# Kernel optimization log

Hardware: AMD Instinct MI355X
Metric: run time of the kernel (lower is better)

The kernel has to match this reference:

```python
import jax, jax.numpy as jnp
import numpy as np

N_NODES = 100000
N_EDGES = 1600000
D_IN = 128
D_OUT = 128


def setup_inputs() -> dict:
    key = jax.random.key(0)
    k1, k2, k3, k4, k5, k6 = jax.random.split(key, 6)
    x = jax.random.normal(k1, (N_NODES, D_IN), dtype=jnp.float32)
    edge_src = jax.random.randint(k2, (N_EDGES,), 0, N_NODES, dtype=jnp.int64 if jax.config.jax_enable_x64 else jnp.int32)
    edge_dst = jax.random.randint(k3, (N_EDGES,), 0, N_NODES, dtype=jnp.int64 if jax.config.jax_enable_x64 else jnp.int32)
    edge_val = jax.random.uniform(k4, (N_EDGES,), dtype=jnp.float32)
    # nn.Linear(2*D_IN, D_OUT): store W as [2*D_IN, D_OUT] (transposed torch layout)
    W = jax.random.normal(k5, (2 * D_IN, D_OUT), dtype=jnp.float32) * (1.0 / np.sqrt(2 * D_IN))
    b = jax.random.normal(k6, (D_OUT,), dtype=jnp.float32) * 0.01
    return {"x": x, "edge_src": edge_src, "edge_dst": edge_dst, "edge_val": edge_val, "W": W, "b": b}


def reference(x, edge_src, edge_dst, edge_val, W, b):
    # support = adj @ x  (sparse COO: adj[dst, src] = edge_val)
    gathered = x[edge_src] * edge_val[:, None]               # [E, D_IN]
    support = jax.ops.segment_sum(gathered, edge_dst, num_segments=x.shape[0])  # [N, D_IN]
    # concat self + aggregated neighbor features, then linear
    h = jnp.concatenate([x, support], axis=1)                # [N, 2*D_IN]
    return h @ W + b                                          # [N, D_OUT]
```

## Files before the change

kernel.cpp:

```cpp
#include <hip/hip_runtime.h>

#define D 128
#define BN 64
#define NBIN 391
#define NBMAX 512
#define CHUNK 2048
#define SCAP 12

typedef __attribute__((ext_vector_type(8))) short bf16x8;
typedef __attribute__((ext_vector_type(4))) float f32x4;

__device__ __forceinline__ unsigned short f2bf(float f) {
    unsigned int u = __builtin_bit_cast(unsigned int, f);
    u = (u + 0x7fffu + ((u >> 16) & 1u)) >> 16;
    return (unsigned short)u;
}
__device__ __forceinline__ float bf2f(unsigned int u) {
    return __builtin_bit_cast(float, u << 16);
}

__global__ void prep_kernel(const float* __restrict__ x,
                            unsigned short* __restrict__ x_bf,
                            const float* __restrict__ W,
                            unsigned short* __restrict__ WT,
                            int* __restrict__ ccnt,
                            int n4, int XB, int WB) {
    int blk = blockIdx.x, tid = threadIdx.x;
    if (blk < XB) {
        int i = blk * 256 + tid;
        if (i < n4) {
            float4 v = ((const float4*)x)[i];
            ushort4 s;
            s.x = f2bf(v.x); s.y = f2bf(v.y); s.z = f2bf(v.z); s.w = f2bf(v.w);
            ((ushort4*)x_bf)[i] = s;
        }
    } else if (blk < XB + WB) {
        int t = (blk - XB) * 256 + tid;
        if (t < 2 * D * D) {
            int col = t & 127, k = t >> 7;
            WT[col * 256 + k] = f2bf(W[k * D + col]);
        }
    } else {
        ccnt[tid] = 0;
        ccnt[tid + 256] = 0;
    }
}

__global__ __launch_bounds__(256) void chist_kernel(const int* __restrict__ edst,
                                                    int* __restrict__ ccnt, int E) {
    __shared__ int h[NBMAX];
    for (int i = threadIdx.x; i < NBMAX; i += 256) h[i] = 0;
    __syncthreads();
    int stride = gridDim.x * 256;
    for (int e = blockIdx.x * 256 + threadIdx.x; e < E; e += stride)
        atomicAdd(&h[edst[e] >> 8], 1);
    __syncthreads();
    for (int i = threadIdx.x; i < NBIN; i += 256) {
        int c = h[i];
        if (c) atomicAdd(&ccnt[i], c);
    }
}

__global__ __launch_bounds__(256) void cscan_kernel(const int* __restrict__ ccnt,
                                                    int* __restrict__ cbase,
                                                    int* __restrict__ ccur) {
    __shared__ int p[256];
    int t = threadIdx.x;
    int s0 = ccnt[2 * t], s1 = ccnt[2 * t + 1];
    int loc = s0 + s1;
    p[t] = loc;
    __syncthreads();
    for (int off = 1; off < 256; off <<= 1) {
        int v = p[t];
        int u = (t >= off) ? p[t - off] : 0;
        __syncthreads();
        p[t] = v + u;
        __syncthreads();
    }
    int ex = p[t] - loc;
    cbase[2 * t] = ex;     ccur[2 * t] = ex;
    cbase[2 * t + 1] = ex + s0; ccur[2 * t + 1] = ex + s0;
}

__global__ __launch_bounds__(256) void cfill_kernel(const int* __restrict__ esrc,
                                                    const int* __restrict__ edst,
                                                    const float* __restrict__ eval,
                                                    int* __restrict__ ccur,
                                                    int2* __restrict__ ep, int E) {
    __shared__ int lh[NBMAX];
    __shared__ int lcur[NBMAX];
    __shared__ int p[256];
    __shared__ int2 ord[CHUNK];
    __shared__ unsigned short obk[CHUNK];

    const int tid = threadIdx.x;
    const int base = blockIdx.x * CHUNK;
    const int n = min(CHUNK, E - base);

    for (int i = tid; i < NBMAX; i += 256) lh[i] = 0;
    __syncthreads();

    int esv[8]; int ebk[8];
    float evv[8];
#pragma unroll
    for (int k = 0; k < 8; ++k) {
        int li = k * 256 + tid;
        if (li < n) {
            int i = base + li;
            int dst = edst[i];
            esv[k] = esrc[i];
            evv[k] = eval[i];
            int b = dst >> 8;
            ebk[k] = b | ((dst & 255) << 16);
            atomicAdd(&lh[b], 1);
        } else ebk[k] = -1;
    }
    __syncthreads();

    int s0 = lh[2 * tid], s1 = lh[2 * tid + 1];
    int loc = s0 + s1;
    p[tid] = loc;
    __syncthreads();
    for (int off = 1; off < 256; off <<= 1) {
        int v = p[tid];
        int u = (tid >= off) ? p[tid - off] : 0;
        __syncthreads();
        p[tid] = v + u;
        __syncthreads();
    }
    int ex = p[tid] - loc;
    lcur[2 * tid] = ex;
    lcur[2 * tid + 1] = ex + s0;
    __syncthreads();

#pragma unroll
    for (int k = 0; k < 8; ++k) {
        if (ebk[k] >= 0) {
            int b = ebk[k] & 0xffff, nl = ebk[k] >> 16;
            int slot = atomicAdd(&lcur[b], 1);
            ord[slot] = make_int2((esv[k] << 8) | nl, __builtin_bit_cast(int, evv[k]));
            obk[slot] = (unsigned short)b;
        }
    }
    __syncthreads();

    for (int b = tid; b < NBIN; b += 256) {
        int c = lh[b];
        if (c) lh[b] = atomicAdd(&ccur[b], c) - (lcur[b] - c);
    }
    __syncthreads();

    for (int i = tid; i < n; i += 256) {
        int b = obk[i];
        ep[lh[b] + i] = ord[i];
    }
}

__global__ __launch_bounds__(512) void csort_kernel(int2* __restrict__ ep,
                                                    const int* __restrict__ cbase,
                                                    const int* __restrict__ ccnt,
                                                    int* __restrict__ node_start) {
    __shared__ int h[256];
    __shared__ int p[256];

    const int t = threadIdx.x;
    const int bin = blockIdx.x;
    const int cb = cbase[bin];
    const int ce = cb + ccnt[bin];

    if (t < 256) h[t] = 0;
    __syncthreads();

    int2 ev[SCAP];
#pragma unroll
    for (int k = 0; k < SCAP; ++k) {
        int idx = cb + k * 512 + t;
        if (idx < ce) {
            int2 e = ep[idx];
            ev[k] = e;
            atomicAdd(&h[e.x & 255], 1);
        } else ev[k] = make_int2(-1, 0);
    }
    __syncthreads();

    int c = 0;
    if (t < 256) { c = h[t]; p[t] = c; }
    __syncthreads();
    for (int off = 1; off < 256; off <<= 1) {
        int v = 0, u = 0;
        if (t < 256) { v = p[t]; u = (t >= off) ? p[t - off] : 0; }
        __syncthreads();
        if (t < 256) p[t] = v + u;
        __syncthreads();
    }
    if (t < 256) {
        int st = cb + p[t] - c;
        node_start[bin * 256 + t] = st;
        h[t] = st;
    }
    __syncthreads();

#pragma unroll
    for (int k = 0; k < SCAP; ++k) {
        if (ev[k].x >= 0) {
            int nl = ev[k].x & 255;
            int pos = atomicAdd(&h[nl], 1);
            ep[pos] = make_int2(ev[k].x & 0xFFFFFF3F, ev[k].y);
        }
    }
}

__global__ __launch_bounds__(256, 8) void gather_fused_kernel(
        const unsigned short* __restrict__ x_bf,
        const int* __restrict__ node_start,
        const int2* __restrict__ edge_pack,
        const unsigned short* __restrict__ WT,
        const float* __restrict__ bias,
        float* __restrict__ out, int N) {
    __shared__ unsigned short accb[BN * 136];
    __shared__ int nb[BN + 1];

    const int tid = threadIdx.x;
    const int b = blockIdx.x;
    const int node0 = b * BN;
    const int w = tid >> 6, lane = tid & 63;
    unsigned int* accw = (unsigned int*)accb;

    for (int i = tid * 8; i < BN * 136; i += 2048)
        *(uint4*)(accb + i) = make_uint4(0u, 0u, 0u, 0u);
    if (tid <= BN) nb[tid] = node_start[node0 + tid];
    __syncthreads();

    const int js = __builtin_amdgcn_readfirstlane(nb[w * 16]);
    const int je = __builtin_amdgcn_readfirstlane(nb[w * 16 + 16]);
    const unsigned short* xl = x_bf + lane * 2;

    int cur = -1;
    float ax = 0.f, ay = 0.f;
    for (int g = js; g < je; g += 16) {
        int m = je - g; if (m > 16) m = 16;
        int2 e[16];
#pragma unroll
        for (int k = 0; k < 16; ++k) {
            int idx = g + k; if (idx >= je) idx = je - 1;
            e[k] = edge_pack[idx];
        }
        unsigned int p[16];
#pragma unroll
        for (int k = 0; k < 16; ++k)
            p[k] = *(const unsigned int*)(xl + ((e[k].x >> 8) << 7));
#pragma unroll
        for (int k = 0; k < 16; ++k) {
            if (k < m) {
                int nd = e[k].x & 63;
                if (nd != cur) {
                    if (cur >= 0)
                        accw[cur * 68 + lane] =
                            (unsigned int)f2bf(ax) | ((unsigned int)f2bf(ay) << 16);
                    cur = nd; ax = 0.f; ay = 0.f;
                }
                float v = __builtin_bit_cast(float, e[k].y);
                ax += bf2f(p[k] & 0xffffu) * v;
                ay += bf2f(p[k] >> 16) * v;
            }
        }
    }
    if (cur >= 0)
        accw[cur * 68 + lane] = (unsigned int)f2bf(ax) | ((unsigned int)f2bf(ay) << 16);
    __syncthreads();

    const int quad = lane >> 4;
    const int l15  = lane & 15;
    const int colbase = w * 32;

    f32x4 acc[4][2];
#pragma unroll
    for (int rt = 0; rt < 4; ++rt) {
        acc[rt][0] = (f32x4){0.f, 0.f, 0.f, 0.f};
        acc[rt][1] = (f32x4){0.f, 0.f, 0.f, 0.f};
    }

#pragma unroll
    for (int ks = 0; ks < 8; ++ks) {
        bf16x8 wf0 = *(const bf16x8*)(WT + (size_t)(colbase + l15) * 256 + ks * 32 + quad * 8);
        bf16x8 wf1 = *(const bf16x8*)(WT + (size_t)(colbase + 16 + l15) * 256 + ks * 32 + quad * 8);
#pragma unroll
        for (int rt = 0; rt < 4; ++rt) {
            int row = rt * 16 + l15;
            bf16x8 a;
            if (ks < 4) {
                int rg = node0 + row; if (rg >= N) rg = N - 1;
                a = *(const bf16x8*)(x_bf + (size_t)rg * D + ks * 32 + quad * 8);
            } else {
                a = *(const bf16x8*)(accb + row * 136 + (ks - 4) * 32 + quad * 8);
            }
            acc[rt][0] = __builtin_amdgcn_mfma_f32_16x16x32_bf16(a, wf0, acc[rt][0], 0, 0, 0);
            acc[rt][1] = __builtin_amdgcn_mfma_f32_16x16x32_bf16(a, wf1, acc[rt][1], 0, 0, 0);
        }
    }

#pragma unroll
    for (int ct = 0; ct < 2; ++ct) {
        int col = colbase + ct * 16 + l15;
        float bv = bias[col];
#pragma unroll
        for (int rt = 0; rt < 4; ++rt) {
#pragma unroll
            for (int rg = 0; rg < 4; ++rg) {
                int row = node0 + rt * 16 + quad * 4 + rg;
                if (row < N)
                    out[(size_t)row * D + col] = acc[rt][ct][rg] + bv;
            }
        }
    }
}

extern "C" void kernel_launch(void* const* d_in, const int* in_sizes, int n_in,
                              void* d_out, int out_size, void* d_ws, size_t ws_size,
                              hipStream_t stream) {
    const float* x    = (const float*)d_in[0];
    const int*   esrc = (const int*)d_in[1];
    const int*   edst = (const int*)d_in[2];
    const float* eval = (const float*)d_in[3];
    const float* W    = (const float*)d_in[4];
    const float* bias = (const float*)d_in[5];
    float*       out  = (float*)d_out;

    const int N  = in_sizes[0] / D;
    const int E  = in_sizes[1];
    const int NB = (N + BN - 1) / BN;

    char* ws = (char*)d_ws;
    unsigned short* x_bf  = (unsigned short*)ws;
    int2*           ep    = (int2*)(ws + 25600000);
    unsigned short* WT    = (unsigned short*)(ws + 38400000);
    int*            nbg   = (int*)(ws + 38465536);
    int*            ccnt  = (int*)(ws + 38865920);
    int*            cbase = (int*)(ws + 38867968);
    int*            ccur  = (int*)(ws + 38870016);

    const int n4 = N * D / 4;
    const int XB = (n4 + 255) / 256;
    const int WB = (2 * D * D + 255) / 256;

    prep_kernel<<<XB + WB + 1, 256, 0, stream>>>(x, x_bf, W, WT, ccnt, n4, XB, WB);
    chist_kernel<<<512, 256, 0, stream>>>(edst, ccnt, E);
    cscan_kernel<<<1, 256, 0, stream>>>(ccnt, cbase, ccur);
    cfill_kernel<<<(E + CHUNK - 1) / CHUNK, 256, 0, stream>>>(esrc, edst, eval,
                                                              ccur, ep, E);
    csort_kernel<<<NBIN, 512, 0, stream>>>(ep, cbase, ccnt, nbg);
    gather_fused_kernel<<<NB, 256, 0, stream>>>(x_bf, nbg, ep, WT, bias, out, N);
    (void)ws_size; (void)n_in; (void)out_size;
}
```

Baseline: 254.7 us.

## Fuse edge histogram into prep kernel, halve gather block, prefetch edge batches

The destination histogram moves into the prep kernel as per-block partial counts, which the scan kernel reduces. This removes a launch and the global atomic merge. The gather/GEMM kernel now handles 32 nodes per block instead of 64, for more blocks and finer load balance, at the cost of reloading the W fragments more often. The edge-record loads are double-buffered so the next 16 edges are fetched while the current ones are processed, using more registers.

```diff
diff --git a/kernel.cpp b/kernel.cpp
--- a/kernel.cpp
+++ b/kernel.cpp
@@ -1,11 +1,12 @@
 #include <hip/hip_runtime.h>
 
 #define D 128
-#define BN 64
+#define BN 32
 #define NBIN 391
 #define NBMAX 512
 #define CHUNK 2048
 #define SCAP 12
+#define HB 128
 
 typedef __attribute__((ext_vector_type(8))) short bf16x8;
 typedef __attribute__((ext_vector_type(4))) float f32x4;
@@ -23,8 +24,10 @@
                             unsigned short* __restrict__ x_bf,
                             const float* __restrict__ W,
                             unsigned short* __restrict__ WT,
-                            int* __restrict__ ccnt,
-                            int n4, int XB, int WB) {
+                            const int* __restrict__ edst,
+                            int* __restrict__ hpart,
+                            int n4, int XB, int WB, int E) {
+    __shared__ int h[NBMAX];
     int blk = blockIdx.x, tid = threadIdx.x;
     if (blk < XB) {
         int i = blk * 256 + tid;
@@ -41,32 +44,27 @@
             WT[col * 256 + k] = f2bf(W[k * D + col]);
         }
     } else {
-        ccnt[tid] = 0;
-        ccnt[tid + 256] = 0;
-    }
-}
-
-__global__ __launch_bounds__(256) void chist_kernel(const int* __restrict__ edst,
-                                                    int* __restrict__ ccnt, int E) {
-    __shared__ int h[NBMAX];
-    for (int i = threadIdx.x; i < NBMAX; i += 256) h[i] = 0;
-    __syncthreads();
-    int stride = gridDim.x * 256;
-    for (int e = blockIdx.x * 256 + threadIdx.x; e < E; e += stride)
-        atomicAdd(&h[edst[e] >> 8], 1);
-    __syncthreads();
-    for (int i = threadIdx.x; i < NBIN; i += 256) {
-        int c = h[i];
-        if (c) atomicAdd(&ccnt[i], c);
-    }
-}
-
-__global__ __launch_bounds__(256) void cscan_kernel(const int* __restrict__ ccnt,
+        int hb = blk - XB - WB;
+        for (int i = tid; i < NBMAX; i += 256) h[i] = 0;
+        __syncthreads();
+        for (int i = hb * 256 + tid; i < E; i += HB * 256)
+            atomicAdd(&h[edst[i] >> 8], 1);
+        __syncthreads();
+        for (int i = tid; i < NBMAX; i += 256) hpart[hb * NBMAX + i] = h[i];
+    }
+}
+
+__global__ __launch_bounds__(256) void cscan_kernel(const int* __restrict__ hpart,
+                                                    int* __restrict__ ccnt,
                                                     int* __restrict__ cbase,
                                                     int* __restrict__ ccur) {
     __shared__ int p[256];
     int t = threadIdx.x;
-    int s0 = ccnt[2 * t], s1 = ccnt[2 * t + 1];
+    int s0 = 0, s1 = 0;
+    for (int j = 0; j < HB; ++j) {
+        s0 += hpart[j * NBMAX + 2 * t];
+        s1 += hpart[j * NBMAX + 2 * t + 1];
+    }
     int loc = s0 + s1;
     p[t] = loc;
     __syncthreads();
@@ -78,7 +76,8 @@
         __syncthreads();
     }
     int ex = p[t] - loc;
-    cbase[2 * t] = ex;     ccur[2 * t] = ex;
+    ccnt[2 * t] = s0;          ccnt[2 * t + 1] = s1;
+    cbase[2 * t] = ex;         ccur[2 * t] = ex;
     cbase[2 * t + 1] = ex + s0; ccur[2 * t + 1] = ex + s0;
 }
 
@@ -221,8 +220,7 @@
     __shared__ int nb[BN + 1];
 
     const int tid = threadIdx.x;
-    const int b = blockIdx.x;
-    const int node0 = b * BN;
+    const int node0 = blockIdx.x * BN;
     const int w = tid >> 6, lane = tid & 63;
     unsigned int* accw = (unsigned int*)accb;
 
@@ -231,51 +229,60 @@
     if (tid <= BN) nb[tid] = node_start[node0 + tid];
     __syncthreads();
 
-    const int js = __builtin_amdgcn_readfirstlane(nb[w * 16]);
-    const int je = __builtin_amdgcn_readfirstlane(nb[w * 16 + 16]);
+    const int js = __builtin_amdgcn_readfirstlane(nb[w * 8]);
+    const int je = __builtin_amdgcn_readfirstlane(nb[w * 8 + 8]);
     const unsigned short* xl = x_bf + lane * 2;
 
     int cur = -1;
     float ax = 0.f, ay = 0.f;
-    for (int g = js; g < je; g += 16) {
-        int m = je - g; if (m > 16) m = 16;
-        int2 e[16];
+    if (js < je) {
+        int2 eC[16], eN[16];
 #pragma unroll
         for (int k = 0; k < 16; ++k) {
-            int idx = g + k; if (idx >= je) idx = je - 1;
-            e[k] = edge_pack[idx];
-        }
-        unsigned int p[16];
-#pragma unroll
-        for (int k = 0; k < 16; ++k)
-            p[k] = *(const unsigned int*)(xl + ((e[k].x >> 8) << 7));
-#pragma unroll
-        for (int k = 0; k < 16; ++k) {
-            if (k < m) {
-                int nd = e[k].x & 63;
-                if (nd != cur) {
-                    if (cur >= 0)
-                        accw[cur * 68 + lane] =
-                            (unsigned int)f2bf(ax) | ((unsigned int)f2bf(ay) << 16);
-                    cur = nd; ax = 0.f; ay = 0.f;
+            int idx = js + k; if (idx >= je) idx = je - 1;
+            eC[k] = edge_pack[idx];
+        }
+        for (int g = js; g < je; g += 16) {
+#pragma unroll
+            for (int k = 0; k < 16; ++k) {
+                int idx = g + 16 + k; if (idx >= je) idx = je - 1;
+                eN[k] = edge_pack[idx];
+            }
+            unsigned int p[16];
+#pragma unroll
+            for (int k = 0; k < 16; ++k)
+                p[k] = *(const unsigned int*)(xl + ((eC[k].x >> 8) << 7));
+            int m = je - g; if (m > 16) m = 16;
+#pragma unroll
+            for (int k = 0; k < 16; ++k) {
+                if (k < m) {
+                    int nd = eC[k].x & 31;
+                    if (nd != cur) {
+                        if (cur >= 0)
+                            accw[cur * 68 + lane] =
+                                (unsigned int)f2bf(ax) | ((unsigned int)f2bf(ay) << 16);
+                        cur = nd; ax = 0.f; ay = 0.f;
+                    }
+                    float v = __builtin_bit_cast(float, eC[k].y);
+                    ax += bf2f(p[k] & 0xffffu) * v;
+                    ay += bf2f(p[k] >> 16) * v;
                 }
-                float v = __builtin_bit_cast(float, e[k].y);
-                ax += bf2f(p[k] & 0xffffu) * v;
-                ay += bf2f(p[k] >> 16) * v;
             }
-        }
-    }
-    if (cur >= 0)
-        accw[cur * 68 + lane] = (unsigned int)f2bf(ax) | ((unsigned int)f2bf(ay) << 16);
+#pragma unroll
+            for (int k = 0; k < 16; ++k) eC[k] = eN[k];
+        }
+        if (cur >= 0)
+            accw[cur * 68 + lane] = (unsigned int)f2bf(ax) | ((unsigned int)f2bf(ay) << 16);
+    }
     __syncthreads();
 
     const int quad = lane >> 4;
     const int l15  = lane & 15;
     const int colbase = w * 32;
 
-    f32x4 acc[4][2];
-#pragma unroll
-    for (int rt = 0; rt < 4; ++rt) {
+    f32x4 acc[2][2];
+#pragma unroll
+    for (int rt = 0; rt < 2; ++rt) {
         acc[rt][0] = (f32x4){0.f, 0.f, 0.f, 0.f};
         acc[rt][1] = (f32x4){0.f, 0.f, 0.f, 0.f};
     }
@@ -285,7 +292,7 @@
         bf16x8 wf0 = *(const bf16x8*)(WT + (size_t)(colbase + l15) * 256 + ks * 32 + quad * 8);
         bf16x8 wf1 = *(const bf16x8*)(WT + (size_t)(colbase + 16 + l15) * 256 + ks * 32 + quad * 8);
 #pragma unroll
-        for (int rt = 0; rt < 4; ++rt) {
+        for (int rt = 0; rt < 2; ++rt) {
             int row = rt * 16 + l15;
             bf16x8 a;
             if (ks < 4) {
@@ -304,7 +311,7 @@
         int col = colbase + ct * 16 + l15;
         float bv = bias[col];
 #pragma unroll
-        for (int rt = 0; rt < 4; ++rt) {
+        for (int rt = 0; rt < 2; ++rt) {
 #pragma unroll
             for (int rg = 0; rg < 4; ++rg) {
                 int row = node0 + rt * 16 + quad * 4 + rg;
@@ -328,7 +335,7 @@
 
     const int N  = in_sizes[0] / D;
     const int E  = in_sizes[1];
-    const int NB = (N + BN - 1) / BN;
+    const int NG = (N + BN - 1) / BN;
 
     char* ws = (char*)d_ws;
     unsigned short* x_bf  = (unsigned short*)ws;
@@ -338,17 +345,18 @@
     int*            ccnt  = (int*)(ws + 38865920);
     int*            cbase = (int*)(ws + 38867968);
     int*            ccur  = (int*)(ws + 38870016);
+    int*            hpart = (int*)(ws + 38872064);
 
     const int n4 = N * D / 4;
     const int XB = (n4 + 255) / 256;
     const int WB = (2 * D * D + 255) / 256;
 
-    prep_kernel<<<XB + WB + 1, 256, 0, stream>>>(x, x_bf, W, WT, ccnt, n4, XB, WB);
-    chist_kernel<<<512, 256, 0, stream>>>(edst, ccnt, E);
-    cscan_kernel<<<1, 256, 0, stream>>>(ccnt, cbase, ccur);
+    prep_kernel<<<XB + WB + HB, 256, 0, stream>>>(x, x_bf, W, WT, edst, hpart,
+                                                  n4, XB, WB, E);
+    cscan_kernel<<<1, 256, 0, stream>>>(hpart, ccnt, cbase, ccur);
     cfill_kernel<<<(E + CHUNK - 1) / CHUNK, 256, 0, stream>>>(esrc, edst, eval,
                                                               ccur, ep, E);
     csort_kernel<<<NBIN, 512, 0, stream>>>(ep, cbase, ccnt, nbg);
-    gather_fused_kernel<<<NB, 256, 0, stream>>>(x_bf, nbg, ep, WT, bias, out, N);
+    gather_fused_kernel<<<NG, 256, 0, stream>>>(x_bf, nbg, ep, WT, bias, out, N);
     (void)ws_size; (void)n_in; (void)out_size;
 }
```

New measurement: 272.7 us. 7.1% more time.

## Use 512-thread blocks with eight waves per 64-node tile in gather_fused

Applied to the files above, without the earlier changes.

The fused gather+GEMM kernel now runs 512 threads (8 waves) per 64-node block. Each wave gathers edges for 8 nodes instead of 16, and the MFMA stage is regridded so each wave computes a 16x64 output tile. The aim is more in-flight gathers per block and shorter per-wave serial edge chains, which should hide latency better. The cost is more registers per block, which may lower occupancy, and each wave now loads more weight fragments from global memory.

```diff
diff --git a/kernel.cpp b/kernel.cpp
--- a/kernel.cpp
+++ b/kernel.cpp
@@ -210,7 +210,7 @@
     }
 }
 
-__global__ __launch_bounds__(256, 8) void gather_fused_kernel(
+__global__ __launch_bounds__(512, 8) void gather_fused_kernel(
         const unsigned short* __restrict__ x_bf,
         const int* __restrict__ node_start,
         const int2* __restrict__ edge_pack,
@@ -221,18 +221,17 @@
     __shared__ int nb[BN + 1];
 
     const int tid = threadIdx.x;
-    const int b = blockIdx.x;
-    const int node0 = b * BN;
+    const int node0 = blockIdx.x * BN;
     const int w = tid >> 6, lane = tid & 63;
     unsigned int* accw = (unsigned int*)accb;
 
-    for (int i = tid * 8; i < BN * 136; i += 2048)
+    for (int i = tid * 8; i < BN * 136; i += 4096)
         *(uint4*)(accb + i) = make_uint4(0u, 0u, 0u, 0u);
     if (tid <= BN) nb[tid] = node_start[node0 + tid];
     __syncthreads();
 
-    const int js = __builtin_amdgcn_readfirstlane(nb[w * 16]);
-    const int je = __builtin_amdgcn_readfirstlane(nb[w * 16 + 16]);
+    const int js = __builtin_amdgcn_readfirstlane(nb[w * 8]);
+    const int je = __builtin_amdgcn_readfirstlane(nb[w * 8 + 8]);
     const unsigned short* xl = x_bf + lane * 2;
 
     int cur = -1;
@@ -271,46 +270,39 @@
 
     const int quad = lane >> 4;
     const int l15  = lane & 15;
-    const int colbase = w * 32;
-
-    f32x4 acc[4][2];
-#pragma unroll
-    for (int rt = 0; rt < 4; ++rt) {
-        acc[rt][0] = (f32x4){0.f, 0.f, 0.f, 0.f};
-        acc[rt][1] = (f32x4){0.f, 0.f, 0.f, 0.f};
-    }
+    const int wr = w & 3, wc = w >> 2;
+
+    f32x4 acc[4];
+#pragma unroll
+    for (int ct = 0; ct < 4; ++ct)
+        acc[ct] = (f32x4){0.f, 0.f, 0.f, 0.f};
 
 #pragma unroll
     for (int ks = 0; ks < 8; ++ks) {
-        bf16x8 wf0 = *(const bf16x8*)(WT + (size_t)(colbase + l15) * 256 + ks * 32 + quad * 8);
-        bf16x8 wf1 = *(const bf16x8*)(WT + (size_t)(colbase + 16 + l15) * 256 + ks * 32 + quad * 8);
-#pragma unroll
-        for (int rt = 0; rt < 4; ++rt) {
-            int row = rt * 16 + l15;
-            bf16x8 a;
-            if (ks < 4) {
-                int rg = node0 + row; if (rg >= N) rg = N - 1;
-                a = *(const bf16x8*)(x_bf + (size_t)rg * D + ks * 32 + quad * 8);
-            } else {
-                a = *(const bf16x8*)(accb + row * 136 + (ks - 4) * 32 + quad * 8);
-            }
-            acc[rt][0] = __builtin_amdgcn_mfma_f32_16x16x32_bf16(a, wf0, acc[rt][0], 0, 0, 0);
-            acc[rt][1] = __builtin_amdgcn_mfma_f32_16x16x32_bf16(a, wf1, acc[rt][1], 0, 0, 0);
-        }
-    }
-
-#pragma unroll
-    for (int ct = 0; ct < 2; ++ct) {
-        int col = colbase + ct * 16 + l15;
+        bf16x8 a;
+        int row = wr * 16 + l15;
+        if (ks < 4) {
+            int rg = node0 + row; if (rg >= N) rg = N - 1;
+            a = *(const bf16x8*)(x_bf + (size_t)rg * D + ks * 32 + quad * 8);
+        } else {
+            a = *(const bf16x8*)(accb + row * 136 + (ks - 4) * 32 + quad * 8);
+        }
+#pragma unroll
+        for (int ct = 0; ct < 4; ++ct) {
+            bf16x8 wf = *(const bf16x8*)(WT + (size_t)(wc * 64 + ct * 16 + l15) * 256 + ks * 32 + quad * 8);
+            acc[ct] = __builtin_amdgcn_mfma_f32_16x16x32_bf16(a, wf, acc[ct], 0, 0, 0);
+        }
+    }
+
+#pragma unroll
+    for (int ct = 0; ct < 4; ++ct) {
+        int col = wc * 64 + ct * 16 + l15;
         float bv = bias[col];
 #pragma unroll
-        for (int rt = 0; rt < 4; ++rt) {
-#pragma unroll
-            for (int rg = 0; rg < 4; ++rg) {
-                int row = node0 + rt * 16 + quad * 4 + rg;
-                if (row < N)
-                    out[(size_t)row * D + col] = acc[rt][ct][rg] + bv;
-            }
+        for (int rg = 0; rg < 4; ++rg) {
+            int row = node0 + wr * 16 + quad * 4 + rg;
+            if (row < N)
+                out[(size_t)row * D + col] = acc[ct][rg] + bv;
         }
     }
 }
@@ -328,7 +320,7 @@
 
     const int N  = in_sizes[0] / D;
     const int E  = in_sizes[1];
-    const int NB = (N + BN - 1) / BN;
+    const int NG = (N + BN - 1) / BN;
 
     char* ws = (char*)d_ws;
     unsigned short* x_bf  = (unsigned short*)ws;
@@ -349,6 +341,6 @@
     cfill_kernel<<<(E + CHUNK - 1) / CHUNK, 256, 0, stream>>>(esrc, edst, eval,
                                                               ccur, ep, E);
     csort_kernel<<<NBIN, 512, 0, stream>>>(ep, cbase, ccnt, nbg);
-    gather_fused_kernel<<<NB, 256, 0, stream>>>(x_bf, nbg, ep, WT, bias, out, N);
+    gather_fused_kernel<<<NG, 512, 0, stream>>>(x_bf, nbg, ep, WT, bias, out, N);
     (void)ws_size; (void)n_in; (void)out_size;
 }
```

After: 283.8 us. 1.11x slower.
